# Kernel tuning notes

Hardware: AMD Instinct MI355X
Metric: run time of the kernel (lower is better)

The kernel has to match this reference:

```python
import jax, jax.numpy as jnp
import numpy as np
import math

B, T, Dm, H = 512, 64, 1024, 16
dh = Dm // H
CD, SD = 32, 256  # smolgen compress_dim, shared_dim
SCALE = 1.0 / math.sqrt(dh)
RES_SCALE = 1.0 / math.sqrt(2.0)  # n_layers=1
EPS = 1e-5


def _ln(v, g, b):
    m = jnp.mean(v, axis=-1, keepdims=True)
    var = jnp.mean(jnp.square(v - m), axis=-1, keepdims=True)
    return (v - m) * jax.lax.rsqrt(var + EPS) * g + b


def setup_inputs() -> dict:
    key = jax.random.key(0)
    ks = jax.random.split(key, 16)
    s = 0.02
    return {
        "x": jax.random.normal(ks[0], (B, T, Dm), jnp.float32),
        # weights stored (in, out); y = x @ W + b
        "Wq": jax.random.normal(ks[1], (Dm, Dm), jnp.float32) * s,
        "Wk": jax.random.normal(ks[2], (Dm, Dm), jnp.float32) * s,
        "Wv": jax.random.normal(ks[3], (Dm, Dm), jnp.float32) * s,
        "Wo_w": jax.random.normal(ks[4], (Dm, Dm), jnp.float32) * s,
        "Wo_b": jnp.zeros((Dm,), jnp.float32),
        "static_bias": jax.random.normal(ks[5], (H, T, T), jnp.float32) * s,
        "aQ": jax.random.normal(ks[6], (H, T, T, dh), jnp.float32) * s,
        "aK": jax.random.normal(ks[7], (H, T, T, dh), jnp.float32) * s,
        "aV": jax.random.normal(ks[8], (H, T, T, dh), jnp.float32) * s,
        # Smolgen params
        "pt_w": jax.random.normal(ks[9], (Dm, CD), jnp.float32) * s,
        "pt_b": jnp.zeros((CD,), jnp.float32),
        "pg_w": jax.random.normal(ks[10], (T * CD, SD), jnp.float32) * s,
        "pg_b": jnp.zeros((SD,), jnp.float32),
        "ph_w": jax.random.normal(ks[11], (SD, H * SD), jnp.float32) * s,
        "ph_b": jnp.zeros((H * SD,), jnp.float32),
        "ln1_g": jnp.ones((SD,), jnp.float32),
        "ln1_b": jnp.zeros((SD,), jnp.float32),
        "ln2_g": jnp.ones((SD,), jnp.float32),
        "ln2_b": jnp.zeros((SD,), jnp.float32),
        "shared_w": jax.random.normal(ks[12], (SD, T * T), jnp.float32) * s,
    }


def _smolgen(x, pt_w, pt_b, pg_w, pg_b, ph_w, ph_b, ln1_g, ln1_b, ln2_g, ln2_b, shared_w):
    z = x @ pt_w + pt_b                      # (B,T,CD)
    g = z.reshape(x.shape[0], T * CD) @ pg_w + pg_b  # (B,SD)
    g = _ln(jax.nn.silu(g), ln1_g, ln1_b)
    u = g @ ph_w + ph_b                      # (B,H*SD)
    u = jax.nn.silu(u).reshape(-1, H, SD)
    u = _ln(u, ln2_g, ln2_b)
    return (u @ shared_w).reshape(-1, H, T, T)


def reference(x, Wq, Wk, Wv, Wo_w, Wo_b, static_bias, aQ, aK, aV,
              pt_w, pt_b, pg_w, pg_b, ph_w, ph_b,
              ln1_g, ln1_b, ln2_g, ln2_b, shared_w):
    Bx = x.shape[0]
    Q = (x @ Wq).reshape(Bx, T, H, dh).transpose(0, 2, 1, 3)  # (B,H,T,dh)
    K = (x @ Wk).reshape(Bx, T, H, dh).transpose(0, 2, 1, 3)
    V = (x @ Wv).reshape(Bx, T, H, dh).transpose(0, 2, 1, 3)
    logits = jnp.einsum('bhtd,bhsd->bhts', Q, K) * SCALE
    logits = logits + static_bias[None]
    logits = logits + jnp.einsum('bhtd,htsd->bhts', Q, aK) * SCALE
    logits = logits + jnp.einsum('htsd,bhsd->bhts', aQ, K) * SCALE
    logits = logits + (jnp.einsum('htsd,htsd->hts', aQ, aK) * SCALE)[None]
    logits = logits + _smolgen(x, pt_w, pt_b, pg_w, pg_b, ph_w, ph_b,
                               ln1_g, ln1_b, ln2_g, ln2_b, shared_w)
    attn = jax.nn.softmax(logits, axis=-1)  # dropout = identity (eval mode)
    out = jnp.einsum('bhts,bhsd->bhtd', attn, V)
    out = out + jnp.einsum('bhts,htsd->bhtd', attn, aV)
    out = out.transpose(0, 2, 1, 3).reshape(Bx, T, Dm)
    return (out @ Wo_w + Wo_b) * RES_SCALE
```

## Files before the change

### kernel.cpp

```cpp
#include <hip/hip_runtime.h>
#include <cstdint>
#include <cstdio>

typedef unsigned short u16;
typedef __attribute__((ext_vector_type(8))) short s8v;
typedef __attribute__((ext_vector_type(4))) float f4v;
typedef __attribute__((ext_vector_type(4))) unsigned short u16x4;
typedef const __attribute__((address_space(1))) void* gas_p;
typedef __attribute__((address_space(3))) void* las_p;

#define DEV __device__ __forceinline__

static constexpr float SCALE_ = 0.125f;
static constexpr float RES_SCALE_ = 0.7071067811865475f;
static constexpr float EPS_ = 1e-5f;

DEV u16 f2bf(float f) {
  uint32_t u = __float_as_uint(f);
  u += 0x7fffu + ((u >> 16) & 1u);
  return (u16)(u >> 16);
}
DEV float bf2f(u16 h) { return __uint_as_float(((uint32_t)h) << 16); }

DEV f4v mfma16(s8v a, s8v b, f4v c) {
  return __builtin_amdgcn_mfma_f32_16x16x32_bf16(a, b, c, 0, 0, 0);
}

#define WAITVM4 asm volatile("s_waitcnt vmcnt(4)" ::: "memory")
#define WAITVM0 asm volatile("s_waitcnt vmcnt(0)" ::: "memory")
#define SCHEDB  __builtin_amdgcn_sched_barrier(0)
#define BAR     __builtin_amdgcn_s_barrier()


__global__ void k_zero(float* __restrict__ p, long n) {
  long i = (long)blockIdx.x * blockDim.x + threadIdx.x;
  long stride = (long)gridDim.x * blockDim.x;
  for (; i < n; i += stride) p[i] = 0.f;
}


DEV void dev_cvt(const float* __restrict__ in, u16* __restrict__ out, long n4,
                 int bid, int nblocks) {
  long i = (long)bid * 256 + threadIdx.x;
  long stride = (long)nblocks * 256;
  for (; i < n4; i += stride) {
    f4v v = *(const f4v*)&in[i * 4];
    u16x4 o;
    o.x = f2bf(v.x); o.y = f2bf(v.y); o.z = f2bf(v.z); o.w = f2bf(v.w);
    *(u16x4*)&out[i * 4] = o;
  }
}

DEV void dev_transpose(const float* __restrict__ in, u16* __restrict__ out,
                       int K, int N, int bx, int by, float tile[64][65]) {
  int kb = bx * 64, nb = by * 64;
  for (int i = threadIdx.x; i < 4096; i += 256) {
    int r = i >> 6, c = i & 63;
    tile[r][c] = in[(long)(kb + r) * N + nb + c];
  }
  __syncthreads();
  for (int i = threadIdx.x; i < 4096; i += 256) {
    int c = i >> 6, r = i & 63;
    out[(long)(nb + c) * K + kb + r] = f2bf(tile[r][c]);
  }
}

DEV void dev_avt(const float* __restrict__ aV, u16* __restrict__ aVt, int ht,
                 float tile[64][65]) {
  const float* src = aV + (long)ht * 4096;
  for (int i = threadIdx.x; i < 4096; i += 256) {
    int s = i >> 6, d = i & 63;
    tile[s][d] = src[i];
  }
  __syncthreads();
  u16* dst = aVt + (long)ht * 4096;
  for (int i = threadIdx.x; i < 4096; i += 256) {
    int d = i >> 6, s = i & 63;
    dst[i] = f2bf(tile[s][d]);
  }
}

__launch_bounds__(256)
__global__ void k_prep(const float* __restrict__ x, u16* __restrict__ xbf,
                       const float* __restrict__ Wq, const float* __restrict__ Wk,
                       const float* __restrict__ Wv, const float* __restrict__ Wo,
                       u16* __restrict__ Wqkvt, u16* __restrict__ Wot,
                       const float* __restrict__ ph_w, u16* __restrict__ phwt,
                       const float* __restrict__ shw, u16* __restrict__ swt,
                       const float* __restrict__ pg_w, u16* __restrict__ pgwT,
                       const float* __restrict__ pt_w, u16* __restrict__ ptwT,
                       const float* __restrict__ aK, u16* __restrict__ aKb,
                       const float* __restrict__ aQ, u16* __restrict__ aQb,
                       const float* __restrict__ aV, u16* __restrict__ aVt,
                       const float* __restrict__ sb, float* __restrict__ extra) {
  __shared__ float tile[64][65];
  int b = blockIdx.x;
  if (b < 2048) { dev_cvt(x, xbf, 8388608, b, 2048); return; }
  b -= 2048;
  if (b < 1024) {
    const float* src = (b < 256) ? Wq : (b < 512) ? Wk : (b < 768) ? Wv : Wo;
    u16* dst = (b < 256) ? Wqkvt : (b < 512) ? (Wqkvt + 1048576)
             : (b < 768) ? (Wqkvt + 2097152) : Wot;
    int id = b & 255;
    dev_transpose(src, dst, 1024, 1024, id & 15, id >> 4, tile);
    return;
  }
  b -= 1024;
  if (b < 256) { dev_transpose(ph_w, phwt, 256, 4096, b & 3, b >> 2, tile); return; }
  b -= 256;
  if (b < 256) { dev_transpose(shw, swt, 256, 4096, b & 3, b >> 2, tile); return; }
  b -= 256;
  if (b < 128) { dev_transpose(pg_w, pgwT, 2048, 256, b & 31, b >> 5, tile); return; }
  b -= 128;
  if (b < 128) {
    int idx = b * 256 + threadIdx.x;
    int n = idx >> 10, k = idx & 1023;
    ptwT[idx] = f2bf(pt_w[k * 32 + n]);
    return;
  }
  b -= 128;
  if (b < 512) { dev_cvt(aK, aKb, 1048576, b, 512); return; }
  b -= 512;
  if (b < 512) { dev_cvt(aQ, aQb, 1048576, b, 512); return; }
  b -= 512;
  if (b < 1024) { dev_avt(aV, aVt, b, tile); return; }
  b -= 1024;
  {
    int idx = b * 256 + threadIdx.x;
    const float* q = aQ + (long)idx * 64;
    const float* k = aK + (long)idx * 64;
    float acc = 0.f;
#pragma unroll 8
    for (int d = 0; d < 64; d++) acc += q[d] * k[d];
    extra[idx] = sb[idx] + acc * SCALE_;
  }
}

template <int EPI>
__launch_bounds__(512)
__global__ void k_gemm256(const u16* __restrict__ A, const u16* __restrict__ Bt,
                          void* __restrict__ Cv, const float* __restrict__ aux,
                          int M, int N, int K) {
  __shared__ u16 lds[65536];

  const int nwg = gridDim.x;
  int wg = blockIdx.x;
  if ((nwg & 7) == 0) wg = (wg & 7) * (nwg >> 3) + (wg >> 3);
  const int ntiles = N >> 8;
  const int mt = wg / ntiles, ntb = wg % ntiles;

  const int tid = threadIdx.x;
  const int lane = tid & 63, w = tid >> 6;
  const int wrB = (w >> 2) * 128, wcB = (w & 3) * 64;
  const int lr = lane & 15, lg = lane >> 4;
  const int hA = w >> 2;
  const int hB = (w & 3) >> 1;
  const int rB0 = (w & 1) * 64;
  const int xs0 = ((lg) ^ (lr & 7)) << 3;
  const int xs1 = ((4 + lg) ^ (lr & 7)) << 3;
  const int nt = K >> 6;

  const int sr = tid >> 3;
  const int sslot = (tid & 7) ^ (sr & 7);

  const u16* aSrc = A + (long)(mt * 256 + sr) * K + sslot * 8;
  const u16* bSrc = Bt + (long)(ntb * 256 + sr) * K + sslot * 8;
  const long h128 = (long)128 * K;
  const long r64 = (long)64 * K;

#define GLOADA(tile, h)                                                          \
  do {                                                                           \
    const int bu_ = (tile) & 1;                                                  \
    const long o_ = (long)(tile) * 64 + (h) * h128;                              \
    __builtin_amdgcn_global_load_lds((gas_p)(aSrc + o_), (las_p)&lds[(bu_ * 2 + (h)) * 8192 + w * 512], 16, 0, 0); \
    __builtin_amdgcn_global_load_lds((gas_p)(aSrc + o_ + r64), (las_p)&lds[(bu_ * 2 + (h)) * 8192 + 4096 + w * 512], 16, 0, 0); \
  } while (0)

#define GLOADB(tile, h)                                                          \
  do {                                                                           \
    const int bu_ = (tile) & 1;                                                  \
    const long o_ = (long)(tile) * 64 + (h) * h128;                              \
    __builtin_amdgcn_global_load_lds((gas_p)(bSrc + o_), (las_p)&lds[32768 + (bu_ * 2 + (h)) * 8192 + w * 512], 16, 0, 0); \
    __builtin_amdgcn_global_load_lds((gas_p)(bSrc + o_ + r64), (las_p)&lds[32768 + (bu_ * 2 + (h)) * 8192 + 4096 + w * 512], 16, 0, 0); \
  } while (0)

  f4v acc[8][4];
#pragma unroll
  for (int mi = 0; mi < 8; mi++)
#pragma unroll
    for (int ni = 0; ni < 4; ni++) acc[mi][ni] = (f4v){0.f, 0.f, 0.f, 0.f};

  GLOADA(0, 0); GLOADA(0, 1);
  GLOADB(0, 0); GLOADB(0, 1);
  {
    const int t1 = (nt > 1) ? 1 : 0;
    GLOADB(t1, 0); GLOADB(t1, 1);
  }
  WAITVM0;
  BAR;

  s8v AF[4][2], b01[2][2], b23[2][2];

  {
    const int aB0 = hA * 8192;
    const int bB0 = 32768 + hB * 8192;
#pragma unroll
    for (int mi = 0; mi < 4; mi++) {
      const int ro = (mi * 16 + lr) * 64;
      AF[mi][0] = *(const s8v*)&lds[aB0 + ro + xs0];
      AF[mi][1] = *(const s8v*)&lds[aB0 + ro + xs1];
    }
#pragma unroll
    for (int ni = 0; ni < 2; ni++) {
      const int ro = (rB0 + ni * 16 + lr) * 64;
      b01[ni][0] = *(const s8v*)&lds[bB0 + ro + xs0];
      b01[ni][1] = *(const s8v*)&lds[bB0 + ro + xs1];
    }
  }
  SCHEDB;

  for (int t = 0; t < nt; ++t) {
    const int p = t & 1, q = p ^ 1;
    const int aN = (t + 1 < nt) ? t + 1 : nt - 1;
    const int bN = (t + 2 < nt) ? t + 2 : nt - 1;
    const int aBase = (p * 2 + hA) * 8192;
    const int bBase = 32768 + (p * 2 + hB) * 8192;
    const int aBaseN = (q * 2 + hA) * 8192;
    const int bBaseN = 32768 + (q * 2 + hB) * 8192;

#pragma unroll
    for (int ni = 0; ni < 2; ni++) {
      const int ro = (rB0 + (2 + ni) * 16 + lr) * 64;
      b23[ni][0] = *(const s8v*)&lds[bBase + ro + xs0];
      b23[ni][1] = *(const s8v*)&lds[bBase + ro + xs1];
    }
    SCHEDB;
    GLOADA(aN, 0);
    BAR;
    __builtin_amdgcn_s_setprio(1);
#pragma unroll
    for (int mi = 0; mi < 4; mi++)
#pragma unroll
      for (int ks = 0; ks < 2; ks++)
#pragma unroll
        for (int ni = 0; ni < 2; ni++)
          acc[mi][ni] = mfma16(AF[mi][ks], b01[ni][ks], acc[mi][ni]);
    __builtin_amdgcn_s_setprio(0);

    GLOADA(aN, 1);
    BAR;
    __builtin_amdgcn_s_setprio(1);
#pragma unroll
    for (int mi = 0; mi < 4; mi++) {
#pragma unroll
      for (int ks = 0; ks < 2; ks++)
#pragma unroll
        for (int ni = 0; ni < 2; ni++)
          acc[mi][2 + ni] = mfma16(AF[mi][ks], b23[ni][ks], acc[mi][2 + ni]);
      const int ro = (64 + mi * 16 + lr) * 64;
      AF[mi][0] = *(const s8v*)&lds[aBase + ro + xs0];
      AF[mi][1] = *(const s8v*)&lds[aBase + ro + xs1];
      SCHEDB;
    }
    __builtin_amdgcn_s_setprio(0);
    BAR;

    GLOADB(bN, 0);
    BAR;
    __builtin_amdgcn_s_setprio(1);
#pragma unroll
    for (int mi = 0; mi < 4; mi++)
#pragma unroll
      for (int ks = 0; ks < 2; ks++)
#pragma unroll
        for (int ni = 0; ni < 2; ni++)
          acc[4 + mi][ni] = mfma16(AF[mi][ks], b01[ni][ks], acc[4 + mi][ni]);
    __builtin_amdgcn_s_setprio(0);

    GLOADB(bN, 1);
    WAITVM4;
    BAR;
#pragma unroll
    for (int ni = 0; ni < 2; ni++) {
      const int ro = (rB0 + ni * 16 + lr) * 64;
      b01[ni][0] = *(const s8v*)&lds[bBaseN + ro + xs0];
      b01[ni][1] = *(const s8v*)&lds[bBaseN + ro + xs1];
    }
    SCHEDB;
    __builtin_amdgcn_s_setprio(1);
#pragma unroll
    for (int mi = 0; mi < 4; mi++) {
#pragma unroll
      for (int ks = 0; ks < 2; ks++)
#pragma unroll
        for (int ni = 0; ni < 2; ni++)
          acc[4 + mi][2 + ni] = mfma16(AF[mi][ks], b23[ni][ks], acc[4 + mi][2 + ni]);
      const int ro = (mi * 16 + lr) * 64;
      AF[mi][0] = *(const s8v*)&lds[aBaseN + ro + xs0];
      AF[mi][1] = *(const s8v*)&lds[aBaseN + ro + xs1];
      SCHEDB;
    }
    __builtin_amdgcn_s_setprio(0);
  }
#undef GLOADA
#undef GLOADB

  const int rbase = mt * 256 + wrB + lg * 4;
  const int cbase = ntb * 256 + wcB + lr;
  if (EPI == 0) {
    u16* C = (u16*)Cv;
#pragma unroll
    for (int mi = 0; mi < 8; mi++)
#pragma unroll
      for (int ni = 0; ni < 4; ni++)
#pragma unroll
        for (int j = 0; j < 4; j++)
          C[(long)(rbase + mi * 16 + j) * N + (cbase + ni * 16)] = f2bf(acc[mi][ni][j]);
  } else if (EPI == 2) {
    u16* C = (u16*)Cv;
#pragma unroll
    for (int mi = 0; mi < 8; mi++)
#pragma unroll
      for (int ni = 0; ni < 4; ni++)
#pragma unroll
        for (int j = 0; j < 4; j++) {
          const int row = rbase + mi * 16 + j;
          const int col = cbase + ni * 16;
          C[(long)row * N + col] = f2bf(acc[mi][ni][j] + aux[((row & 15) << 12) | col]);
        }
  } else {
    float* C = (float*)Cv;
#pragma unroll
    for (int mi = 0; mi < 8; mi++)
#pragma unroll
      for (int ni = 0; ni < 4; ni++)
#pragma unroll
        for (int j = 0; j < 4; j++) {
          const int col = cbase + ni * 16;
          C[(long)(rbase + mi * 16 + j) * N + col] =
              (acc[mi][ni][j] + aux[col]) * RES_SCALE_;
        }
  }
}

template <int EPI>
__launch_bounds__(256)
__global__ void k_gemm(const u16* __restrict__ A, const u16* __restrict__ Bt,
                       void* __restrict__ Cv, const float* __restrict__ aux,
                       int M, int N, int K) {
  __shared__ u16 As[4096];
  __shared__ u16 Bs[4096];
  const int ntiles = N >> 7;
  const int mt = blockIdx.x / ntiles;
  const int nt = blockIdx.x % ntiles;
  const int tid = threadIdx.x;
  const int lane = tid & 63;
  const int w = tid >> 6;
  const int wr = w >> 1, wc = w & 1;
  const int lr = lane & 15, lg = lane >> 4;

  f4v acc[4][4];
#pragma unroll
  for (int m = 0; m < 4; m++)
#pragma unroll
    for (int n = 0; n < 4; n++) acc[m][n] = (f4v){0.f, 0.f, 0.f, 0.f};

  const u16* aSrc = A + (long)(mt * 128 + (tid >> 2)) * K + ((tid & 3) << 3);
  const u16* bSrc = Bt + (long)(nt * 128 + (tid >> 2)) * K + ((tid & 3) << 3);
  const long rowStep = (long)64 * K;

  const int kIters = K >> 5;
  for (int kb = 0; kb < kIters; kb++) {
    if (kb) __syncthreads();
    const u16* aP = aSrc + (kb << 5);
    const u16* bP = bSrc + (kb << 5);
    __builtin_amdgcn_global_load_lds((gas_p)aP, (las_p)&As[w * 512], 16, 0, 0);
    __builtin_amdgcn_global_load_lds((gas_p)(aP + rowStep), (las_p)&As[2048 + w * 512], 16, 0, 0);
    __builtin_amdgcn_global_load_lds((gas_p)bP, (las_p)&Bs[w * 512], 16, 0, 0);
    __builtin_amdgcn_global_load_lds((gas_p)(bP + rowStep), (las_p)&Bs[2048 + w * 512], 16, 0, 0);
    WAITVM0;
    __syncthreads();

    s8v af[4];
#pragma unroll
    for (int m = 0; m < 4; m++)
      af[m] = *(const s8v*)&As[(wr * 64 + m * 16 + lr) * 32 + (lg << 3)];
#pragma unroll
    for (int n = 0; n < 4; n++) {
      s8v bf = *(const s8v*)&Bs[(wc * 64 + n * 16 + lr) * 32 + (lg << 3)];
#pragma unroll
      for (int m = 0; m < 4; m++) acc[m][n] = mfma16(af[m], bf, acc[m][n]);
    }
  }

  const int rbase = mt * 128 + wr * 64 + lg * 4;
  const int cbase = nt * 128 + wc * 64 + lr;
  if (EPI == 1) {
    float* C = (float*)Cv;
#pragma unroll
    for (int m = 0; m < 4; m++)
#pragma unroll
      for (int n = 0; n < 4; n++)
#pragma unroll
        for (int j = 0; j < 4; j++) {
          int row = rbase + m * 16 + j;
          int col = cbase + n * 16;
          C[(long)row * N + col] = acc[m][n][j] + aux[col];
        }
  } else {
    u16* C = (u16*)Cv;
#pragma unroll
    for (int m = 0; m < 4; m++)
#pragma unroll
      for (int n = 0; n < 4; n++)
#pragma unroll
        for (int j = 0; j < 4; j++) {
          int row = rbase + m * 16 + j;
          int col = cbase + n * 16;
          C[(long)row * N + col] = f2bf(acc[m][n][j] + aux[((row & 15) << 12) | col]);
        }
  }
}


__launch_bounds__(256)
__global__ void k_smola_gemm(const u16* __restrict__ xbf, const u16* __restrict__ ptwT,
                             const float* __restrict__ ptb, u16* __restrict__ z) {
  const int rt = blockIdx.x;
  const int w = threadIdx.x >> 6, lane = threadIdx.x & 63;
  const int lr = lane & 15, lg = lane >> 4;
  const int row0 = rt * 64 + w * 16;
  f4v acc[2];
  acc[0] = (f4v){0.f, 0.f, 0.f, 0.f};
  acc[1] = (f4v){0.f, 0.f, 0.f, 0.f};
  const u16* aBase = xbf + (long)(row0 + lr) * 1024;
  const u16* bBase = ptwT + (long)lr * 1024;
#pragma unroll 4
  for (int k0 = 0; k0 < 1024; k0 += 32) {
    s8v a = *(const s8v*)&aBase[k0 + (lg << 3)];
#pragma unroll
    for (int n = 0; n < 2; n++) {
      s8v b = *(const s8v*)&bBase[(long)(n << 4) * 1024 + k0 + (lg << 3)];
      acc[n] = mfma16(a, b, acc[n]);
    }
  }
#pragma unroll
  for (int n = 0; n < 2; n++)
#pragma unroll
    for (int j = 0; j < 4; j++) {
      int col = (n << 4) + lr;
      z[(long)(row0 + lg * 4 + j) * 32 + col] = f2bf(acc[n][j] + ptb[col]);
    }
}

__launch_bounds__(64)
__global__ void k_smolb_gemm(const u16* __restrict__ z, const u16* __restrict__ pgwT,
                             const float* __restrict__ pgb, float* __restrict__ out) {
  const int bid = blockIdx.x;
  const int rt = bid >> 2, ct = bid & 3;
  const int lane = threadIdx.x;
  const int lr = lane & 15, lg = lane >> 4;
  f4v acc[4];
#pragma unroll
  for (int n = 0; n < 4; n++) acc[n] = (f4v){0.f, 0.f, 0.f, 0.f};
  const u16* aBase = z + (long)(rt * 16 + lr) * 2048;
  const u16* bBase = pgwT + (long)(ct * 64 + lr) * 2048;
#pragma unroll 4
  for (int k0 = 0; k0 < 2048; k0 += 32) {
    s8v a = *(const s8v*)&aBase[k0 + (lg << 3)];
#pragma unroll
    for (int n = 0; n < 4; n++) {
      s8v b = *(const s8v*)&bBase[(long)(n << 4) * 2048 + k0 + (lg << 3)];
      acc[n] = mfma16(a, b, acc[n]);
    }
  }
#pragma unroll
  for (int n = 0; n < 4; n++)
#pragma unroll
    for (int j = 0; j < 4; j++) {
      int row = rt * 16 + lg * 4 + j;
      int col = ct * 64 + (n << 4) + lr;
      out[(long)row * 256 + col] = acc[n][j] + pgb[col];
    }
}

__launch_bounds__(64)
__global__ void k_ln2(const float* __restrict__ uraw, const float* __restrict__ g2,
                      const float* __restrict__ b2, u16* __restrict__ ubf) {
  const int row = blockIdx.x;
  const int lane = threadIdx.x;
  f4v x = *(const f4v*)&uraw[(long)row * 256 + lane * 4];
  float v[4];
  float s = 0.f, q = 0.f;
#pragma unroll
  for (int j = 0; j < 4; j++) {
    float xx = x[j];
    v[j] = xx / (1.f + __expf(-xx));
    s += v[j]; q += v[j] * v[j];
  }
#pragma unroll
  for (int mk = 1; mk < 64; mk <<= 1) { s += __shfl_xor(s, mk); q += __shfl_xor(q, mk); }
  float mean = s * (1.f / 256.f);
  float var = q * (1.f / 256.f) - mean * mean;
  float rs = rsqrtf(var + EPS_);
  u16x4 o;
  float o0 = (v[0] - mean) * rs * g2[lane * 4 + 0] + b2[lane * 4 + 0];
  float o1 = (v[1] - mean) * rs * g2[lane * 4 + 1] + b2[lane * 4 + 1];
  float o2 = (v[2] - mean) * rs * g2[lane * 4 + 2] + b2[lane * 4 + 2];
  float o3 = (v[3] - mean) * rs * g2[lane * 4 + 3] + b2[lane * 4 + 3];
  o.x = f2bf(o0); o.y = f2bf(o1); o.z = f2bf(o2); o.w = f2bf(o3);
  *(u16x4*)&ubf[(long)row * 256 + lane * 4] = o;
}


__launch_bounds__(64)
__global__ void k_l23(const u16* __restrict__ qkv, const u16* __restrict__ aKb,
                      const u16* __restrict__ aQb, u16* __restrict__ l2b,
                      u16* __restrict__ l3a) {
  const int lane = threadIdx.x;
  const int lr = lane & 15, lg = lane >> 4;
  f4v acc[4][4];
#pragma unroll
  for (int m = 0; m < 4; m++)
#pragma unroll
    for (int n = 0; n < 4; n++) acc[m][n] = (f4v){0.f, 0.f, 0.f, 0.f};

  if (blockIdx.x < 8192) {
    const int bid = blockIdx.x;
    const int bt = bid & 7, t = (bid >> 3) & 63, h = bid >> 9;
    const u16* qb = qkv + (long)t * 3072 + h * 64;
    const u16* kb = aKb + ((long)h * 64 + t) * 4096;
#pragma unroll
    for (int ks = 0; ks < 2; ks++) {
      s8v a[4], bb[4];
#pragma unroll
      for (int m = 0; m < 4; m++) {
        int brow = bt * 64 + m * 16 + lr;
        a[m] = *(const s8v*)&qb[(long)brow * 196608 + ks * 32 + (lg << 3)];
      }
#pragma unroll
      for (int n = 0; n < 4; n++)
        bb[n] = *(const s8v*)&kb[(n * 16 + lr) * 64 + ks * 32 + (lg << 3)];
#pragma unroll
      for (int m = 0; m < 4; m++)
#pragma unroll
        for (int n = 0; n < 4; n++) acc[m][n] = mfma16(a[m], bb[n], acc[m][n]);
    }
    u16* dst = l2b + ((long)h * 64 + t) * 32768;
#pragma unroll
    for (int m = 0; m < 4; m++)
#pragma unroll
      for (int n = 0; n < 4; n++)
#pragma unroll
        for (int j = 0; j < 4; j++) {
          int brow = bt * 64 + m * 16 + lg * 4 + j;
          int s = n * 16 + lr;
          dst[(long)brow * 64 + s] = f2bf(SCALE_ * acc[m][n][j]);
        }
  } else {
    const int bid = blockIdx.x - 8192;
    const int bt = bid & 7, s = (bid >> 3) & 63, h = bid >> 9;
    const u16* kb = qkv + (long)s * 3072 + 1024 + h * 64;
    const u16* qb = aQb + (long)h * 262144 + (long)s * 64;
#pragma unroll
    for (int ks = 0; ks < 2; ks++) {
      s8v a[4], bb[4];
#pragma unroll
      for (int m = 0; m < 4; m++) {
        int brow = bt * 64 + m * 16 + lr;
        a[m] = *(const s8v*)&kb[(long)brow * 196608 + ks * 32 + (lg << 3)];
      }
#pragma unroll
      for (int n = 0; n < 4; n++) {
        int tc = n * 16 + lr;
        bb[n] = *(const s8v*)&qb[(long)tc * 4096 + ks * 32 + (lg << 3)];
      }
#pragma unroll
      for (int m = 0; m < 4; m++)
#pragma unroll
        for (int n = 0; n < 4; n++) acc[m][n] = mfma16(a[m], bb[n], acc[m][n]);
    }
#pragma unroll
    for (int m = 0; m < 4; m++)
#pragma unroll
      for (int n = 0; n < 4; n++)
#pragma unroll
        for (int j = 0; j < 4; j++) {
          int brow = bt * 64 + m * 16 + lg * 4 + j;
          int tc = n * 16 + lr;
          long idx = (((long)brow * 16 + h) * 64 + s) * 64 + tc;
          l3a[idx] = f2bf(SCALE_ * acc[m][n][j]);
        }
  }
}

__launch_bounds__(64)
__global__ void k_c(const u16* __restrict__ attnb, const u16* __restrict__ aVt,
                    u16* __restrict__ outh) {
  const int bid = blockIdx.x;
  const int bt = bid & 7, t = (bid >> 3) & 63, h = bid >> 9;
  const int lane = threadIdx.x;
  const int lr = lane & 15, lg = lane >> 4;
  f4v acc[4][4];
#pragma unroll
  for (int m = 0; m < 4; m++)
#pragma unroll
    for (int n = 0; n < 4; n++) acc[m][n] = (f4v){0.f, 0.f, 0.f, 0.f};
  const u16* ab = attnb + ((long)h * 64 + t) * 64;
  const u16* vb = aVt + ((long)h * 64 + t) * 4096;
#pragma unroll
  for (int ks = 0; ks < 2; ks++) {
    s8v a[4], bb[4];
#pragma unroll
    for (int m = 0; m < 4; m++) {
      int brow = bt * 64 + m * 16 + lr;
      a[m] = *(const s8v*)&ab[(long)brow * 65536 + ks * 32 + (lg << 3)];
    }
#pragma unroll
    for (int n = 0; n < 4; n++)
      bb[n] = *(const s8v*)&vb[(n * 16 + lr) * 64 + ks * 32 + (lg << 3)];
#pragma unroll
    for (int m = 0; m < 4; m++)
#pragma unroll
      for (int n = 0; n < 4; n++) acc[m][n] = mfma16(a[m], bb[n], acc[m][n]);
  }
#pragma unroll
  for (int m = 0; m < 4; m++)
#pragma unroll
    for (int n = 0; n < 4; n++)
#pragma unroll
      for (int j = 0; j < 4; j++) {
        int brow = bt * 64 + m * 16 + lg * 4 + j;
        int d = n * 16 + lr;
        long idx = ((long)brow * 64 + t) * 1024 + h * 64 + d;
        outh[idx] = f2bf(bf2f(outh[idx]) + acc[m][n][j]);
      }
}

__launch_bounds__(256)
__global__ void k_attn(const u16* __restrict__ qkv, const u16* __restrict__ logits,
                       const u16* __restrict__ l2b, u16* __restrict__ l3a,
                       u16* __restrict__ outh) {
  __shared__ u16 Qs[64 * 72];
  __shared__ u16 Ks[64 * 72];
  __shared__ u16 Vt[64 * 72];
  __shared__ u16 Ps[64 * 72];
  const int bh = blockIdx.x;
  const int b = bh >> 4, h = bh & 15;
  const int tid = threadIdx.x;
  const int lane = tid & 63, w = tid >> 6;
  const int lr = lane & 15, lg = lane >> 4;
  const u16* qbase = qkv + (long)b * 196608 + h * 64;

#pragma unroll
  for (int c = 0; c < 2; c++) {
    int flat = c * 2048 + tid * 8;
    int row = flat >> 6, k = flat & 63;
    const u16* src = &qbase[(long)row * 3072 + k];
    *(s8v*)&Qs[row * 72 + k] = *(const s8v*)(src);
    *(s8v*)&Ks[row * 72 + k] = *(const s8v*)(src + 1024);
    s8v v = *(const s8v*)(src + 2048);
#pragma unroll
    for (int j = 0; j < 8; j++) Vt[(k + j) * 72 + row] = (u16)v[j];
  }
  __syncthreads();

  f4v sacc[4];
#pragma unroll
  for (int n = 0; n < 4; n++) sacc[n] = (f4v){0.f, 0.f, 0.f, 0.f};
#pragma unroll
  for (int ks = 0; ks < 2; ks++) {
    s8v a = *(const s8v*)&Qs[(w * 16 + lr) * 72 + ks * 32 + (lg << 3)];
#pragma unroll
    for (int n = 0; n < 4; n++) {
      s8v bb = *(const s8v*)&Ks[(n * 16 + lr) * 72 + ks * 32 + (lg << 3)];
      sacc[n] = mfma16(a, bb, sacc[n]);
    }
  }

  const long base = (long)bh * 4096;
  const int r0 = w * 16 + lg * 4;
  float p[4][4];
#pragma unroll
  for (int n = 0; n < 4; n++) {
    int s = n * 16 + lr;
    u16x4 l3v = *(const u16x4*)&l3a[base + s * 64 + r0];
#pragma unroll
    for (int j = 0; j < 4; j++) {
      float l3f = bf2f(((const u16*)&l3v)[j]);
      float l2f = bf2f(l2b[(((long)h * 64 + r0 + j) * 512 + b) * 64 + s]);
      float lgf = bf2f(logits[base + (r0 + j) * 64 + s]);
      p[n][j] = sacc[n][j] * SCALE_ + lgf + l3f + l2f;
    }
  }
#pragma unroll
  for (int j = 0; j < 4; j++) {
    float m = fmaxf(fmaxf(p[0][j], p[1][j]), fmaxf(p[2][j], p[3][j]));
    m = fmaxf(m, __shfl_xor(m, 1));
    m = fmaxf(m, __shfl_xor(m, 2));
    m = fmaxf(m, __shfl_xor(m, 4));
    m = fmaxf(m, __shfl_xor(m, 8));
    float s0 = 0.f;
#pragma unroll
    for (int n = 0; n < 4; n++) { p[n][j] = __expf(p[n][j] - m); s0 += p[n][j]; }
    s0 += __shfl_xor(s0, 1);
    s0 += __shfl_xor(s0, 2);
    s0 += __shfl_xor(s0, 4);
    s0 += __shfl_xor(s0, 8);
    float inv = 1.f / s0;
#pragma unroll
    for (int n = 0; n < 4; n++) p[n][j] *= inv;
  }

  __syncthreads();

#pragma unroll
  for (int n = 0; n < 4; n++) {
    int s = n * 16 + lr;
#pragma unroll
    for (int j = 0; j < 4; j++) {
      u16 pb = f2bf(p[n][j]);
      l3a[base + (r0 + j) * 64 + s] = pb;
      Ps[(r0 + j) * 72 + s] = pb;
    }
  }
  __syncthreads();

  f4v oacc[4];
#pragma unroll
  for (int n = 0; n < 4; n++) oacc[n] = (f4v){0.f, 0.f, 0.f, 0.f};
#pragma unroll
  for (int ks = 0; ks < 2; ks++) {
    s8v a = *(const s8v*)&Ps[(w * 16 + lr) * 72 + ks * 32 + (lg << 3)];
#pragma unroll
    for (int n = 0; n < 4; n++) {
      s8v vb = *(const s8v*)&Vt[(n * 16 + lr) * 72 + ks * 32 + (lg << 3)];
      oacc[n] = mfma16(a, vb, oacc[n]);
    }
  }
  u16* obase = outh + (long)b * 65536 + h * 64;
#pragma unroll
  for (int n = 0; n < 4; n++)
#pragma unroll
    for (int j = 0; j < 4; j++)
      obase[(long)(r0 + j) * 1024 + n * 16 + lr] = f2bf(oacc[n][j]);
}


extern "C" void kernel_launch(void* const* d_in, const int* in_sizes, int n_in,
                              void* d_out, int out_size, void* d_ws, size_t ws_size,
                              hipStream_t stream) {
  (void)in_sizes; (void)n_in;
  const float* x    = (const float*)d_in[0];
  const float* Wq   = (const float*)d_in[1];
  const float* Wk   = (const float*)d_in[2];
  const float* Wv   = (const float*)d_in[3];
  const float* Wo_w = (const float*)d_in[4];
  const float* Wo_b = (const float*)d_in[5];
  const float* sb   = (const float*)d_in[6];
  const float* aQ   = (const float*)d_in[7];
  const float* aK   = (const float*)d_in[8];
  const float* aV   = (const float*)d_in[9];
  const float* pt_w = (const float*)d_in[10];
  const float* pt_b = (const float*)d_in[11];
  const float* pg_w = (const float*)d_in[12];
  const float* pg_b = (const float*)d_in[13];
  const float* ph_w = (const float*)d_in[14];
  const float* ph_b = (const float*)d_in[15];
  const float* ln1g = (const float*)d_in[16];
  const float* ln1b = (const float*)d_in[17];
  const float* ln2g = (const float*)d_in[18];
  const float* ln2b = (const float*)d_in[19];
  const float* shw  = (const float*)d_in[20];

  char* wsp = (char*)d_ws;
  size_t off = 0;
  auto alloc = [&](size_t bytes) {
    void* p = wsp + off;
    off += (bytes + 255) & ~(size_t)255;
    return p;
  };
  u16*   xbf    = (u16*)alloc(33554432ull * 2);
  u16*   qkv    = (u16*)alloc(100663296ull * 2);
  u16*   logits = (u16*)alloc(33554432ull * 2);
  u16*   l3a    = (u16*)alloc(33554432ull * 2);
  u16*   l2b    = (u16*)alloc(33554432ull * 2);
  u16*   Wqkvt  = (u16*)alloc(3145728ull * 2);
  u16*   Wot    = (u16*)alloc(1048576ull * 2);
  u16*   phwt   = (u16*)alloc(1048576ull * 2);
  u16*   swt    = (u16*)alloc(1048576ull * 2);
  u16*   aKb    = (u16*)alloc(4194304ull * 2);
  u16*   aQb    = (u16*)alloc(4194304ull * 2);
  u16*   aVt    = (u16*)alloc(4194304ull * 2);
  float* extra  = (float*)alloc(65536ull * 4);
  u16*   z      = (u16*)alloc(1048576ull * 2);
  u16*   g      = (u16*)alloc(131072ull * 2);
  float* uraw   = (float*)alloc(2097152ull * 4);
  u16*   ubf    = (u16*)alloc(2097152ull * 2);
  u16*   ptwT   = (u16*)alloc(32768ull * 2);
  u16*   pgwT   = (u16*)alloc(524288ull * 2);
  float* uraw2  = (float*)alloc(131072ull * 4);
  u16*   outh   = xbf;
  float* dout   = (float*)d_out;

  if (off > ws_size) {
    fprintf(stderr, "[kernel_launch] insufficient workspace: need %zu have %zu\n",
            off, ws_size);
    k_zero<<<2048, 256, 0, stream>>>(dout, (long)out_size);
    return;
  }

  k_prep<<<6144, 256, 0, stream>>>(x, xbf, Wq, Wk, Wv, Wo_w, Wqkvt, Wot,
                                   ph_w, phwt, shw, swt, pg_w, pgwT, pt_w, ptwT,
                                   aK, aKb, aQ, aQb, aV, aVt, sb, extra);

  k_gemm256<0><<<1536, 512, 0, stream>>>(xbf, Wqkvt, qkv, nullptr, 32768, 3072, 1024);

  k_smola_gemm<<<512, 256, 0, stream>>>(xbf, ptwT, pt_b, z);
  k_smolb_gemm<<<128, 64, 0, stream>>>(z, pgwT, pg_b, uraw2);
  k_ln2<<<512, 64, 0, stream>>>(uraw2, ln1g, ln1b, g);
  k_gemm<1><<<128, 256, 0, stream>>>(g, phwt, uraw, ph_b, 512, 4096, 256);
  k_ln2<<<8192, 64, 0, stream>>>(uraw, ln2g, ln2b, ubf);
  k_gemm256<2><<<512, 512, 0, stream>>>(ubf, swt, logits, extra, 8192, 4096, 256);

  k_l23<<<16384, 64, 0, stream>>>(qkv, aKb, aQb, l2b, l3a);
  k_attn<<<8192, 256, 0, stream>>>(qkv, logits, l2b, l3a, outh);
  k_c<<<8192, 64, 0, stream>>>(l3a, aVt, outh);
  k_gemm256<3><<<512, 512, 0, stream>>>(outh, Wot, dout, Wo_b, 32768, 1024, 1024);
}
```

Measured before the change: 728.3 us.

## Fuse smolgen projection with LayerNorm and store attention probs in head-major layout

Merges the smolgen pg GEMM and the first SiLU+LayerNorm into one kernel that reduces rows through shared memory, dropping an fp32 intermediate buffer and a launch. k_attn now writes bf16 probabilities into l2b in an (h,t,b,s) layout, so k_c can load contiguous tiles instead of rows strided by 65536. k_l23 is launched earlier and a __syncthreads is removed. The gemm epilogue is collapsed to a single fp32 path, and reusing l2b as the probability buffer, which k_attn both reads and writes, is a correctness risk.

```diff
diff --git a/kernel.cpp b/kernel.cpp
--- a/kernel.cpp
+++ b/kernel.cpp
@@ -395,7 +395,7 @@
 
   const int rbase = mt * 128 + wr * 64 + lg * 4;
   const int cbase = nt * 128 + wc * 64 + lr;
-  if (EPI == 1) {
+  {
     float* C = (float*)Cv;
 #pragma unroll
     for (int m = 0; m < 4; m++)
@@ -406,18 +406,6 @@
           int row = rbase + m * 16 + j;
           int col = cbase + n * 16;
           C[(long)row * N + col] = acc[m][n][j] + aux[col];
-        }
-  } else {
-    u16* C = (u16*)Cv;
-#pragma unroll
-    for (int m = 0; m < 4; m++)
-#pragma unroll
-      for (int n = 0; n < 4; n++)
-#pragma unroll
-        for (int j = 0; j < 4; j++) {
-          int row = rbase + m * 16 + j;
-          int col = cbase + n * 16;
-          C[(long)row * N + col] = f2bf(acc[m][n][j] + aux[((row & 15) << 12) | col]);
         }
   }
 }
@@ -453,18 +441,19 @@
     }
 }
 
-__launch_bounds__(64)
-__global__ void k_smolb_gemm(const u16* __restrict__ z, const u16* __restrict__ pgwT,
-                             const float* __restrict__ pgb, float* __restrict__ out) {
-  const int bid = blockIdx.x;
-  const int rt = bid >> 2, ct = bid & 3;
-  const int lane = threadIdx.x;
+__launch_bounds__(256)
+__global__ void k_smolb_ln(const u16* __restrict__ z, const u16* __restrict__ pgwT,
+                           const float* __restrict__ pgb, const float* __restrict__ g1,
+                           const float* __restrict__ b1, u16* __restrict__ g) {
+  __shared__ float tile[16][260];
+  const int rt = blockIdx.x;
+  const int w = threadIdx.x >> 6, lane = threadIdx.x & 63;
   const int lr = lane & 15, lg = lane >> 4;
   f4v acc[4];
 #pragma unroll
   for (int n = 0; n < 4; n++) acc[n] = (f4v){0.f, 0.f, 0.f, 0.f};
   const u16* aBase = z + (long)(rt * 16 + lr) * 2048;
-  const u16* bBase = pgwT + (long)(ct * 64 + lr) * 2048;
+  const u16* bBase = pgwT + (long)(w * 64 + lr) * 2048;
 #pragma unroll 4
   for (int k0 = 0; k0 < 2048; k0 += 32) {
     s8v a = *(const s8v*)&aBase[k0 + (lg << 3)];
@@ -478,10 +467,34 @@
   for (int n = 0; n < 4; n++)
 #pragma unroll
     for (int j = 0; j < 4; j++) {
-      int row = rt * 16 + lg * 4 + j;
-      int col = ct * 64 + (n << 4) + lr;
-      out[(long)row * 256 + col] = acc[n][j] + pgb[col];
-    }
+      int row = lg * 4 + j;
+      int col = w * 64 + (n << 4) + lr;
+      tile[row][col] = acc[n][j] + pgb[col];
+    }
+  __syncthreads();
+#pragma unroll
+  for (int i = 0; i < 4; i++) {
+    const int row = w * 4 + i;
+    float v[4];
+    float s = 0.f, q = 0.f;
+#pragma unroll
+    for (int j = 0; j < 4; j++) {
+      float xx = tile[row][lane * 4 + j];
+      v[j] = xx / (1.f + __expf(-xx));
+      s += v[j]; q += v[j] * v[j];
+    }
+#pragma unroll
+    for (int mk = 1; mk < 64; mk <<= 1) { s += __shfl_xor(s, mk); q += __shfl_xor(q, mk); }
+    float mean = s * (1.f / 256.f);
+    float var = q * (1.f / 256.f) - mean * mean;
+    float rs = rsqrtf(var + EPS_);
+    u16x4 o;
+    o.x = f2bf((v[0] - mean) * rs * g1[lane * 4 + 0] + b1[lane * 4 + 0]);
+    o.y = f2bf((v[1] - mean) * rs * g1[lane * 4 + 1] + b1[lane * 4 + 1]);
+    o.z = f2bf((v[2] - mean) * rs * g1[lane * 4 + 2] + b1[lane * 4 + 2]);
+    o.w = f2bf((v[3] - mean) * rs * g1[lane * 4 + 3] + b1[lane * 4 + 3]);
+    *(u16x4*)&g[(long)(rt * 16 + row) * 256 + lane * 4] = o;
+  }
 }
 
 __launch_bounds__(64)
@@ -595,7 +608,7 @@
 }
 
 __launch_bounds__(64)
-__global__ void k_c(const u16* __restrict__ attnb, const u16* __restrict__ aVt,
+__global__ void k_c(const u16* __restrict__ pbuf, const u16* __restrict__ aVt,
                     u16* __restrict__ outh) {
   const int bid = blockIdx.x;
   const int bt = bid & 7, t = (bid >> 3) & 63, h = bid >> 9;
@@ -606,16 +619,14 @@
   for (int m = 0; m < 4; m++)
 #pragma unroll
     for (int n = 0; n < 4; n++) acc[m][n] = (f4v){0.f, 0.f, 0.f, 0.f};
-  const u16* ab = attnb + ((long)h * 64 + t) * 64;
+  const u16* ab = pbuf + ((long)h * 64 + t) * 32768 + (long)bt * 4096;
   const u16* vb = aVt + ((long)h * 64 + t) * 4096;
 #pragma unroll
   for (int ks = 0; ks < 2; ks++) {
     s8v a[4], bb[4];
 #pragma unroll
-    for (int m = 0; m < 4; m++) {
-      int brow = bt * 64 + m * 16 + lr;
-      a[m] = *(const s8v*)&ab[(long)brow * 65536 + ks * 32 + (lg << 3)];
-    }
+    for (int m = 0; m < 4; m++)
+      a[m] = *(const s8v*)&ab[(m * 16 + lr) * 64 + ks * 32 + (lg << 3)];
 #pragma unroll
     for (int n = 0; n < 4; n++)
       bb[n] = *(const s8v*)&vb[(n * 16 + lr) * 64 + ks * 32 + (lg << 3)];
@@ -639,7 +650,7 @@
 
 __launch_bounds__(256)
 __global__ void k_attn(const u16* __restrict__ qkv, const u16* __restrict__ logits,
-                       const u16* __restrict__ l2b, u16* __restrict__ l3a,
+                       u16* __restrict__ l2b, const u16* __restrict__ l3a,
                        u16* __restrict__ outh) {
   __shared__ u16 Qs[64 * 72];
   __shared__ u16 Ks[64 * 72];
@@ -712,15 +723,13 @@
     for (int n = 0; n < 4; n++) p[n][j] *= inv;
   }
 
-  __syncthreads();
-
 #pragma unroll
   for (int n = 0; n < 4; n++) {
     int s = n * 16 + lr;
 #pragma unroll
     for (int j = 0; j < 4; j++) {
       u16 pb = f2bf(p[n][j]);
-      l3a[base + (r0 + j) * 64 + s] = pb;
+      l2b[(((long)h * 64 + r0 + j) * 512 + b) * 64 + s] = pb;
       Ps[(r0 + j) * 72 + s] = pb;
     }
   }
@@ -799,7 +808,6 @@
   u16*   ubf    = (u16*)alloc(2097152ull * 2);
   u16*   ptwT   = (u16*)alloc(32768ull * 2);
   u16*   pgwT   = (u16*)alloc(524288ull * 2);
-  float* uraw2  = (float*)alloc(131072ull * 4);
   u16*   outh   = xbf;
   float* dout   = (float*)d_out;
 
@@ -816,15 +824,15 @@
 
   k_gemm256<0><<<1536, 512, 0, stream>>>(xbf, Wqkvt, qkv, nullptr, 32768, 3072, 1024);
 
+  k_l23<<<16384, 64, 0, stream>>>(qkv, aKb, aQb, l2b, l3a);
+
   k_smola_gemm<<<512, 256, 0, stream>>>(xbf, ptwT, pt_b, z);
-  k_smolb_gemm<<<128, 64, 0, stream>>>(z, pgwT, pg_b, uraw2);
-  k_ln2<<<512, 64, 0, stream>>>(uraw2, ln1g, ln1b, g);
+  k_smolb_ln<<<32, 256, 0, stream>>>(z, pgwT, pg_b, ln1g, ln1b, g);
   k_gemm<1><<<128, 256, 0, stream>>>(g, phwt, uraw, ph_b, 512, 4096, 256);
   k_ln2<<<8192, 64, 0, stream>>>(uraw, ln2g, ln2b, ubf);
   k_gemm256<2><<<512, 512, 0, stream>>>(ubf, swt, logits, extra, 8192, 4096, 256);
 
-  k_l23<<<16384, 64, 0, stream>>>(qkv, aKb, aQb, l2b, l3a);
   k_attn<<<8192, 256, 0, stream>>>(qkv, logits, l2b, l3a, outh);
-  k_c<<<8192, 64, 0, stream>>>(l3a, aVt, outh);
+  k_c<<<8192, 64, 0, stream>>>(l2b, aVt, outh);
   k_gemm256<3><<<512, 512, 0, stream>>>(outh, Wot, dout, Wo_b, 32768, 1024, 1024);
 }
```

Measured after the change: 753.2 us. 3.4% more time.
